# Optimization experiments

Hardware: AMD Instinct MI355X
Metric: run time of the kernel (lower is better)

The kernel has to match this reference:

```python
import jax, jax.numpy as jnp
import numpy as np

N_NODES = 50000
N_EDGES = 1600000
H_DIM = 128
OUT_DIM = 128
N_RELS = 16


def setup_inputs() -> dict:
    key = jax.random.key(0)
    k1, k2, k3, k4, k5, k6 = jax.random.split(key, 6)
    node_ids = jnp.arange(N_NODES, dtype=jnp.int64) if jax.config.jax_enable_x64 else jnp.arange(N_NODES, dtype=jnp.int32)
    src = jax.random.randint(k1, (N_EDGES,), 0, N_NODES, dtype=jnp.int32)
    dst = jax.random.randint(k2, (N_EDGES,), 0, N_NODES, dtype=jnp.int32)
    rel = jax.random.randint(k3, (N_EDGES,), 0, N_RELS, dtype=jnp.int32)
    norm = jax.random.uniform(k4, (N_EDGES, 1), dtype=jnp.float32)
    emb_table = jax.random.normal(k5, (N_NODES, H_DIM), dtype=jnp.float32)
    W = jax.random.normal(k6, (N_RELS, H_DIM, OUT_DIM), dtype=jnp.float32) * (1.0 / np.sqrt(H_DIM))
    return {"node_ids": node_ids, "src": src, "dst": dst, "rel": rel,
            "norm": norm, "emb_table": emb_table, "W": W}


def reference(node_ids, src, dst, rel, norm, emb_table, W):
    # Input layer: embedding lookup on node ids.  [N, h_dim]
    h = emb_table[node_ids]
    n_nodes = emb_table.shape[0]
    # RelGraphConv (full per-relation weight, no basis, no self-loop,
    # activation=None for the single/last layer, dropout inactive at eval):
    # Transform all node features by every relation weight up front
    # (R small, avoids [E, d, o] per-edge weight gather).  [R, N, out]
    h_rel = jnp.einsum('nd,rdo->rno', h, W)
    # Gather per-edge transformed source features, apply edge norm.  [E, out]
    msg = h_rel[rel, src] * norm
    # Scatter-sum messages to destination nodes.  [N, out]
    out = jax.ops.segment_sum(msg, dst, num_segments=n_nodes)
    return out
```

## Files before the change

kernel.cpp:

```cpp
#include <hip/hip_runtime.h>
#include <hip/hip_bf16.h>

#define NN 50000
#define NE 1600000
#define HD 128
#define OD 128
#define NR 16
#define NNP 50176
#define HIST_BLKS 391
#define PREPH_BLKS 6250
#define PREPW_BLKS 1024

typedef __bf16 bf16x8 __attribute__((ext_vector_type(8)));
typedef unsigned short u16x8 __attribute__((ext_vector_type(8)));
typedef float f32x4 __attribute__((ext_vector_type(4)));

__device__ __forceinline__ unsigned short f2bf(float f) {
    union { float f; unsigned int u; } v; v.f = f;
    unsigned int u = v.u;
    u += 0x7FFFu + ((u >> 16) & 1u);
    return (unsigned short)(u >> 16);
}
__device__ __forceinline__ float bflo(unsigned int u) {
    union { unsigned int u; float f; } v; v.u = u << 16; return v.f;
}
__device__ __forceinline__ float bfhi(unsigned int u) {
    union { unsigned int u; float f; } v; v.u = u & 0xFFFF0000u; return v.f;
}

__global__ __launch_bounds__(256) void prep_fused(const int* __restrict__ node_ids,
                                                  const float* __restrict__ emb,
                                                  unsigned short* __restrict__ h_bf,
                                                  const float* __restrict__ W,
                                                  unsigned short* __restrict__ Wt,
                                                  const int* __restrict__ dst,
                                                  int* __restrict__ counts4,
                                                  unsigned short* __restrict__ rank16) {
    const int b = blockIdx.x;
    const int t = threadIdx.x;
    if (b < HIST_BLKS) {
        int t16 = (b * 256 + t) * 16;
        if (t16 >= NE) return;
        int4 d0 = *(const int4*)(dst + t16);
        int4 d1 = *(const int4*)(dst + t16 + 4);
        int4 d2 = *(const int4*)(dst + t16 + 8);
        int4 d3 = *(const int4*)(dst + t16 + 12);
        int r0  = atomicAdd(&counts4[d0.x], 1);
        int r1  = atomicAdd(&counts4[NNP + d0.y], 1);
        int r2  = atomicAdd(&counts4[2 * NNP + d0.z], 1);
        int r3  = atomicAdd(&counts4[3 * NNP + d0.w], 1);
        int r4  = atomicAdd(&counts4[d1.x], 1);
        int r5  = atomicAdd(&counts4[NNP + d1.y], 1);
        int r6  = atomicAdd(&counts4[2 * NNP + d1.z], 1);
        int r7  = atomicAdd(&counts4[3 * NNP + d1.w], 1);
        int r8  = atomicAdd(&counts4[d2.x], 1);
        int r9  = atomicAdd(&counts4[NNP + d2.y], 1);
        int r10 = atomicAdd(&counts4[2 * NNP + d2.z], 1);
        int r11 = atomicAdd(&counts4[3 * NNP + d2.w], 1);
        int r12 = atomicAdd(&counts4[d3.x], 1);
        int r13 = atomicAdd(&counts4[NNP + d3.y], 1);
        int r14 = atomicAdd(&counts4[2 * NNP + d3.z], 1);
        int r15 = atomicAdd(&counts4[3 * NNP + d3.w], 1);
        uint4 pa, pb;
        pa.x = (unsigned int)(r0  & 0xFFFF) | ((unsigned int)r1  << 16);
        pa.y = (unsigned int)(r2  & 0xFFFF) | ((unsigned int)r3  << 16);
        pa.z = (unsigned int)(r4  & 0xFFFF) | ((unsigned int)r5  << 16);
        pa.w = (unsigned int)(r6  & 0xFFFF) | ((unsigned int)r7  << 16);
        pb.x = (unsigned int)(r8  & 0xFFFF) | ((unsigned int)r9  << 16);
        pb.y = (unsigned int)(r10 & 0xFFFF) | ((unsigned int)r11 << 16);
        pb.z = (unsigned int)(r12 & 0xFFFF) | ((unsigned int)r13 << 16);
        pb.w = (unsigned int)(r14 & 0xFFFF) | ((unsigned int)r15 << 16);
        *(uint4*)(rank16 + t16) = pa;
        *(uint4*)(rank16 + t16 + 8) = pb;
    } else if (b < HIST_BLKS + PREPH_BLKS) {
        int gid = (b - HIST_BLKS) * 256 + t;
        int row = gid >> 5;
        int c = (gid & 31) << 2;
        int nid = node_ids[row];
        if (nid < 0) nid = 0; if (nid >= NN) nid = NN - 1;
        float4 v = *(const float4*)(emb + (size_t)nid * HD + c);
        ushort4 o;
        o.x = f2bf(v.x); o.y = f2bf(v.y); o.z = f2bf(v.z); o.w = f2bf(v.w);
        *(ushort4*)(h_bf + (size_t)row * HD + c) = o;
    } else {
        int gid = (b - HIST_BLKS - PREPH_BLKS) * 256 + t;
        int r = gid >> 14;
        int idx = gid & 16383;
        int k = idx >> 7;
        int o = idx & 127;
        Wt[(size_t)r * 16384 + (size_t)o * 128 + k] = f2bf(W[gid]);
    }
}

__global__ __launch_bounds__(256) void gemm_hrel(const unsigned short* __restrict__ h_bf,
                                                 const unsigned short* __restrict__ Wt,
                                                 unsigned short* __restrict__ h_rel) {
    __shared__ unsigned short sA[128][136];
    __shared__ unsigned short sB[128][136];
    const int t = threadIdx.x;
    const int base = blockIdx.x * 128;
    const int rg = blockIdx.y;

    #pragma unroll
    for (int j = 0; j < 8; ++j) {
        int idx = t + j * 256;
        int row = idx >> 4;
        int c8 = (idx & 15) << 3;
        int g = base + row;
        if (g >= NN) g = 0;
        uint4 v = *(const uint4*)(h_bf + (size_t)g * 128 + c8);
        *(uint4*)&sA[row][c8] = v;
    }

    const int lane = t & 63;
    const int w = t >> 6;
    const int wr = w >> 1, wc = w & 1;
    const int l15 = lane & 15, lhi = lane >> 4;

    for (int rr = 0; rr < 4; ++rr) {
        const int r = rg * 4 + rr;
        if (rr > 0) __syncthreads();
        const unsigned short* wp = Wt + ((size_t)r << 14);
        #pragma unroll
        for (int j = 0; j < 8; ++j) {
            int idx = t + j * 256;
            int row = idx >> 4;
            int c8 = (idx & 15) << 3;
            uint4 v = *(const uint4*)(wp + (size_t)row * 128 + c8);
            *(uint4*)&sB[row][c8] = v;
        }
        __syncthreads();

        f32x4 acc[4][4];
        #pragma unroll
        for (int i = 0; i < 4; ++i)
            #pragma unroll
            for (int j = 0; j < 4; ++j)
                acc[i][j] = (f32x4){0.f, 0.f, 0.f, 0.f};

        #pragma unroll
        for (int kt = 0; kt < 4; ++kt) {
            const int ko = kt * 32 + lhi * 8;
            bf16x8 aF[4], bF[4];
            #pragma unroll
            for (int ms = 0; ms < 4; ++ms) {
                u16x8 raw = *(const u16x8*)&sA[wr * 64 + ms * 16 + l15][ko];
                aF[ms] = __builtin_bit_cast(bf16x8, raw);
            }
            #pragma unroll
            for (int nt = 0; nt < 4; ++nt) {
                u16x8 raw = *(const u16x8*)&sB[wc * 64 + nt * 16 + l15][ko];
                bF[nt] = __builtin_bit_cast(bf16x8, raw);
            }
            #pragma unroll
            for (int ms = 0; ms < 4; ++ms)
                #pragma unroll
                for (int nt = 0; nt < 4; ++nt)
                    acc[ms][nt] = __builtin_amdgcn_mfma_f32_16x16x32_bf16(
                        aF[ms], bF[nt], acc[ms][nt], 0, 0, 0);
        }

        #pragma unroll
        for (int ms = 0; ms < 4; ++ms) {
            #pragma unroll
            for (int reg = 0; reg < 4; ++reg) {
                int m = base + wr * 64 + ms * 16 + lhi * 4 + reg;
                if (m < NN) {
                    size_t rowp = ((size_t)r * NN + m) * 128;
                    #pragma unroll
                    for (int nt = 0; nt < 4; ++nt) {
                        int o = wc * 64 + nt * 16 + l15;
                        h_rel[rowp + o] = f2bf(acc[ms][nt][reg]);
                    }
                }
            }
        }
    }
}


__global__ __launch_bounds__(256) void scanA(const int* __restrict__ counts4,
                                             int* __restrict__ blockSums) {
    __shared__ int s[256];
    int t = threadIdx.x;
    int idx = blockIdx.x * 256 + t;
    s[t] = counts4[idx] + counts4[NNP + idx] + counts4[2 * NNP + idx]
         + counts4[3 * NNP + idx];
    __syncthreads();
    for (int off = 128; off > 0; off >>= 1) {
        if (t < off) s[t] += s[t + off];
        __syncthreads();
    }
    if (t == 0) blockSums[blockIdx.x] = s[0];
}

__global__ __launch_bounds__(256) void scanB(int* __restrict__ blockSums) {
    __shared__ int s[256];
    int t = threadIdx.x;
    int v = (t < 196) ? blockSums[t] : 0;
    s[t] = v;
    __syncthreads();
    for (int off = 1; off < 256; off <<= 1) {
        int x = (t >= off) ? s[t - off] : 0;
        __syncthreads();
        s[t] += x;
        __syncthreads();
    }
    if (t < 196) blockSums[t] = s[t] - v;
}

__global__ __launch_bounds__(256) void scanC(int* __restrict__ counts4,
                                             const int* __restrict__ blockSums) {
    __shared__ int s[256];
    int t = threadIdx.x;
    int idx = blockIdx.x * 256 + t;
    int c0 = counts4[idx], c1 = counts4[NNP + idx];
    int c2 = counts4[2 * NNP + idx], c3 = counts4[3 * NNP + idx];
    int v = c0 + c1 + c2 + c3;
    s[t] = v;
    __syncthreads();
    for (int off = 1; off < 256; off <<= 1) {
        int x = (t >= off) ? s[t - off] : 0;
        __syncthreads();
        s[t] += x;
        __syncthreads();
    }
    int st = blockSums[blockIdx.x] + s[t] - v;
    counts4[idx] = st;
    counts4[NNP + idx] = st + c0;
    counts4[2 * NNP + idx] = st + c0 + c1;
    counts4[3 * NNP + idx] = st + c0 + c1 + c2;
}

__global__ __launch_bounds__(256) void scatter_norank(const int* __restrict__ src,
                                                      const int* __restrict__ dst,
                                                      const int* __restrict__ rel,
                                                      const float* __restrict__ norm,
                                                      const int* __restrict__ startS,
                                                      const unsigned short* __restrict__ rank16,
                                                      uint2* __restrict__ recs) {
    int e4 = (blockIdx.x * 256 + threadIdx.x) * 4;
    if (e4 >= NE) return;
    int4 dv = *(const int4*)(dst + e4);
    int4 sv = *(const int4*)(src + e4);
    int4 rv = *(const int4*)(rel + e4);
    float4 nv = *(const float4*)(norm + e4);
    ushort4 rk = *(const ushort4*)(rank16 + e4);
    int p0 = startS[dv.x] + (int)rk.x;
    int p1 = startS[NNP + dv.y] + (int)rk.y;
    int p2 = startS[2 * NNP + dv.z] + (int)rk.z;
    int p3 = startS[3 * NNP + dv.w] + (int)rk.w;
    recs[p0] = make_uint2((unsigned int)(rv.x * NN + sv.x), __float_as_uint(nv.x));
    recs[p1] = make_uint2((unsigned int)(rv.y * NN + sv.y), __float_as_uint(nv.y));
    recs[p2] = make_uint2((unsigned int)(rv.z * NN + sv.z), __float_as_uint(nv.z));
    recs[p3] = make_uint2((unsigned int)(rv.w * NN + sv.w), __float_as_uint(nv.w));
}

__global__ __launch_bounds__(256) void seg_reduce(const int* __restrict__ start,
                                                  const uint2* __restrict__ recs,
                                                  const unsigned int* __restrict__ hb,
                                                  float* __restrict__ out) {
    int d = blockIdx.x * 4 + (threadIdx.x >> 6);
    if (d >= NN) return;
    int lane = threadIdx.x & 63;
    int beg = start[d], end = start[d + 1];
    float a0 = 0.f, a1 = 0.f;
    int i = beg;
    if ((i & 1) && i < end) {
        uint2 rc = recs[i];
        unsigned int u = hb[rc.x * 64u + lane];
        float nm = __uint_as_float(rc.y);
        a0 += bflo(u) * nm;
        a1 += bfhi(u) * nm;
        ++i;
    }
    for (; i + 7 < end; i += 8) {
        uint4 p0 = *(const uint4*)&recs[i];
        uint4 p1 = *(const uint4*)&recs[i + 2];
        uint4 p2 = *(const uint4*)&recs[i + 4];
        uint4 p3 = *(const uint4*)&recs[i + 6];
        unsigned int u0 = hb[p0.x * 64u + lane];
        unsigned int u1 = hb[p0.z * 64u + lane];
        unsigned int u2 = hb[p1.x * 64u + lane];
        unsigned int u3 = hb[p1.z * 64u + lane];
        unsigned int u4 = hb[p2.x * 64u + lane];
        unsigned int u5 = hb[p2.z * 64u + lane];
        unsigned int u6 = hb[p3.x * 64u + lane];
        unsigned int u7 = hb[p3.z * 64u + lane];
        float n0 = __uint_as_float(p0.y), n1 = __uint_as_float(p0.w);
        float n2 = __uint_as_float(p1.y), n3 = __uint_as_float(p1.w);
        float n4 = __uint_as_float(p2.y), n5 = __uint_as_float(p2.w);
        float n6 = __uint_as_float(p3.y), n7 = __uint_as_float(p3.w);
        a0 += bflo(u0) * n0 + bflo(u1) * n1 + bflo(u2) * n2 + bflo(u3) * n3;
        a1 += bfhi(u0) * n0 + bfhi(u1) * n1 + bfhi(u2) * n2 + bfhi(u3) * n3;
        a0 += bflo(u4) * n4 + bflo(u5) * n5 + bflo(u6) * n6 + bflo(u7) * n7;
        a1 += bfhi(u4) * n4 + bfhi(u5) * n5 + bfhi(u6) * n6 + bfhi(u7) * n7;
    }
    for (; i < end; ++i) {
        uint2 rc = recs[i];
        unsigned int u = hb[rc.x * 64u + lane];
        float nm = __uint_as_float(rc.y);
        a0 += bflo(u) * nm;
        a1 += bfhi(u) * nm;
    }
    *(float2*)(out + (size_t)d * 128 + lane * 2) = make_float2(a0, a1);
}


extern "C" void kernel_launch(void* const* d_in, const int* in_sizes, int n_in,
                              void* d_out, int out_size, void* d_ws, size_t ws_size,
                              hipStream_t stream) {
    const int* node_ids = (const int*)d_in[0];
    const int* src      = (const int*)d_in[1];
    const int* dst      = (const int*)d_in[2];
    const int* rel      = (const int*)d_in[3];
    const float* norm   = (const float*)d_in[4];
    const float* emb    = (const float*)d_in[5];
    const float* W      = (const float*)d_in[6];
    float* out = (float*)d_out;

    char* ws = (char*)d_ws;
    unsigned short* h_rel = (unsigned short*)(ws);
    unsigned short* h_bf  = (unsigned short*)(ws + 204800000);
    uint2* recs           = (uint2*)(ws + 204800000);
    unsigned short* Wt    = (unsigned short*)(ws + 217600000);
    int* counts4          = (int*)(ws + 218124288);
    unsigned short* rank16= (unsigned short*)(ws + 218927104);
    int* blockSums        = (int*)(ws + 222127104);

    hipMemsetAsync(counts4, 0, 4 * NNP * sizeof(int), stream);

    prep_fused<<<HIST_BLKS + PREPH_BLKS + PREPW_BLKS, 256, 0, stream>>>(
        node_ids, emb, h_bf, W, Wt, dst, counts4, rank16);
    scanA<<<196, 256, 0, stream>>>(counts4, blockSums);
    scanB<<<1, 256, 0, stream>>>(blockSums);
    scanC<<<196, 256, 0, stream>>>(counts4, blockSums);

    gemm_hrel<<<dim3(391, 4), 256, 0, stream>>>(h_bf, Wt, h_rel);

    scatter_norank<<<(NE / 4 + 255) / 256, 256, 0, stream>>>(src, dst, rel, norm,
                                                             counts4, rank16, recs);

    seg_reduce<<<12500, 256, 0, stream>>>(counts4, recs,
                                          (const unsigned int*)h_rel, out);
}
```

Before: 337.7 us.

## Overlap destination histogram atomics with relation GEMM in one launch

```diff
diff --git a/kernel.cpp b/kernel.cpp
--- a/kernel.cpp
+++ b/kernel.cpp
@@ -7,9 +7,11 @@
 #define OD 128
 #define NR 16
 #define NNP 50176
-#define HIST_BLKS 391
 #define PREPH_BLKS 6250
 #define PREPW_BLKS 1024
+#define HB 64
+#define NCH 100000
+#define GEMM_BLKS 1564
 
 typedef __bf16 bf16x8 __attribute__((ext_vector_type(8)));
 typedef unsigned short u16x8 __attribute__((ext_vector_type(8)));
@@ -28,52 +30,15 @@
     union { unsigned int u; float f; } v; v.u = u & 0xFFFF0000u; return v.f;
 }
 
-__global__ __launch_bounds__(256) void prep_fused(const int* __restrict__ node_ids,
-                                                  const float* __restrict__ emb,
-                                                  unsigned short* __restrict__ h_bf,
-                                                  const float* __restrict__ W,
-                                                  unsigned short* __restrict__ Wt,
-                                                  const int* __restrict__ dst,
-                                                  int* __restrict__ counts4,
-                                                  unsigned short* __restrict__ rank16) {
+__global__ __launch_bounds__(256) void prep_hw(const int* __restrict__ node_ids,
+                                               const float* __restrict__ emb,
+                                               unsigned short* __restrict__ h_bf,
+                                               const float* __restrict__ W,
+                                               unsigned short* __restrict__ Wt) {
     const int b = blockIdx.x;
     const int t = threadIdx.x;
-    if (b < HIST_BLKS) {
-        int t16 = (b * 256 + t) * 16;
-        if (t16 >= NE) return;
-        int4 d0 = *(const int4*)(dst + t16);
-        int4 d1 = *(const int4*)(dst + t16 + 4);
-        int4 d2 = *(const int4*)(dst + t16 + 8);
-        int4 d3 = *(const int4*)(dst + t16 + 12);
-        int r0  = atomicAdd(&counts4[d0.x], 1);
-        int r1  = atomicAdd(&counts4[NNP + d0.y], 1);
-        int r2  = atomicAdd(&counts4[2 * NNP + d0.z], 1);
-        int r3  = atomicAdd(&counts4[3 * NNP + d0.w], 1);
-        int r4  = atomicAdd(&counts4[d1.x], 1);
-        int r5  = atomicAdd(&counts4[NNP + d1.y], 1);
-        int r6  = atomicAdd(&counts4[2 * NNP + d1.z], 1);
-        int r7  = atomicAdd(&counts4[3 * NNP + d1.w], 1);
-        int r8  = atomicAdd(&counts4[d2.x], 1);
-        int r9  = atomicAdd(&counts4[NNP + d2.y], 1);
-        int r10 = atomicAdd(&counts4[2 * NNP + d2.z], 1);
-        int r11 = atomicAdd(&counts4[3 * NNP + d2.w], 1);
-        int r12 = atomicAdd(&counts4[d3.x], 1);
-        int r13 = atomicAdd(&counts4[NNP + d3.y], 1);
-        int r14 = atomicAdd(&counts4[2 * NNP + d3.z], 1);
-        int r15 = atomicAdd(&counts4[3 * NNP + d3.w], 1);
-        uint4 pa, pb;
-        pa.x = (unsigned int)(r0  & 0xFFFF) | ((unsigned int)r1  << 16);
-        pa.y = (unsigned int)(r2  & 0xFFFF) | ((unsigned int)r3  << 16);
-        pa.z = (unsigned int)(r4  & 0xFFFF) | ((unsigned int)r5  << 16);
-        pa.w = (unsigned int)(r6  & 0xFFFF) | ((unsigned int)r7  << 16);
-        pb.x = (unsigned int)(r8  & 0xFFFF) | ((unsigned int)r9  << 16);
-        pb.y = (unsigned int)(r10 & 0xFFFF) | ((unsigned int)r11 << 16);
-        pb.z = (unsigned int)(r12 & 0xFFFF) | ((unsigned int)r13 << 16);
-        pb.w = (unsigned int)(r14 & 0xFFFF) | ((unsigned int)r15 << 16);
-        *(uint4*)(rank16 + t16) = pa;
-        *(uint4*)(rank16 + t16 + 8) = pb;
-    } else if (b < HIST_BLKS + PREPH_BLKS) {
-        int gid = (b - HIST_BLKS) * 256 + t;
+    if (b < PREPH_BLKS) {
+        int gid = b * 256 + t;
         int row = gid >> 5;
         int c = (gid & 31) << 2;
         int nid = node_ids[row];
@@ -83,7 +48,7 @@
         o.x = f2bf(v.x); o.y = f2bf(v.y); o.z = f2bf(v.z); o.w = f2bf(v.w);
         *(ushort4*)(h_bf + (size_t)row * HD + c) = o;
     } else {
-        int gid = (b - HIST_BLKS - PREPH_BLKS) * 256 + t;
+        int gid = (b - PREPH_BLKS) * 256 + t;
         int r = gid >> 14;
         int idx = gid & 16383;
         int k = idx >> 7;
@@ -92,23 +57,69 @@
     }
 }
 
-__global__ __launch_bounds__(256) void gemm_hrel(const unsigned short* __restrict__ h_bf,
-                                                 const unsigned short* __restrict__ Wt,
-                                                 unsigned short* __restrict__ h_rel) {
+__global__ __launch_bounds__(256) void gemm_hist(
+        const unsigned short* __restrict__ h_bf,
+        const unsigned short* __restrict__ Wt,
+        unsigned short* __restrict__ h_rel,
+        const int* __restrict__ dst,
+        int* __restrict__ counts4,
+        unsigned short* __restrict__ rank16) {
     __shared__ unsigned short sA[128][136];
     __shared__ unsigned short sB[128][136];
     const int t = threadIdx.x;
-    const int base = blockIdx.x * 128;
-    const int rg = blockIdx.y;
+
+    if (blockIdx.x < HB) {
+        int tid = blockIdx.x * 256 + t;
+        for (int c = tid; c < NCH; c += HB * 256) {
+            int e16 = c * 16;
+            int4 d0 = *(const int4*)(dst + e16);
+            int4 d1 = *(const int4*)(dst + e16 + 4);
+            int4 d2 = *(const int4*)(dst + e16 + 8);
+            int4 d3 = *(const int4*)(dst + e16 + 12);
+            int r0  = atomicAdd(&counts4[d0.x], 1);
+            int r1  = atomicAdd(&counts4[NNP + d0.y], 1);
+            int r2  = atomicAdd(&counts4[2 * NNP + d0.z], 1);
+            int r3  = atomicAdd(&counts4[3 * NNP + d0.w], 1);
+            int r4  = atomicAdd(&counts4[d1.x], 1);
+            int r5  = atomicAdd(&counts4[NNP + d1.y], 1);
+            int r6  = atomicAdd(&counts4[2 * NNP + d1.z], 1);
+            int r7  = atomicAdd(&counts4[3 * NNP + d1.w], 1);
+            int r8  = atomicAdd(&counts4[d2.x], 1);
+            int r9  = atomicAdd(&counts4[NNP + d2.y], 1);
+            int r10 = atomicAdd(&counts4[2 * NNP + d2.z], 1);
+            int r11 = atomicAdd(&counts4[3 * NNP + d2.w], 1);
+            int r12 = atomicAdd(&counts4[d3.x], 1);
+            int r13 = atomicAdd(&counts4[NNP + d3.y], 1);
+            int r14 = atomicAdd(&counts4[2 * NNP + d3.z], 1);
+            int r15 = atomicAdd(&counts4[3 * NNP + d3.w], 1);
+            uint4 pa, pb;
+            pa.x = (unsigned int)(r0  & 0xFFFF) | ((unsigned int)r1  << 16);
+            pa.y = (unsigned int)(r2  & 0xFFFF) | ((unsigned int)r3  << 16);
+            pa.z = (unsigned int)(r4  & 0xFFFF) | ((unsigned int)r5  << 16);
+            pa.w = (unsigned int)(r6  & 0xFFFF) | ((unsigned int)r7  << 16);
+            pb.x = (unsigned int)(r8  & 0xFFFF) | ((unsigned int)r9  << 16);
+            pb.y = (unsigned int)(r10 & 0xFFFF) | ((unsigned int)r11 << 16);
+            pb.z = (unsigned int)(r12 & 0xFFFF) | ((unsigned int)r13 << 16);
+            pb.w = (unsigned int)(r14 & 0xFFFF) | ((unsigned int)r15 << 16);
+            *(uint4*)(rank16 + e16) = pa;
+            *(uint4*)(rank16 + e16 + 8) = pb;
+        }
+        return;
+    }
+
+    const int g = blockIdx.x - HB;
+    const int tile = g % 391;
+    const int rg = g / 391;
+    const int base = tile * 128;
 
     #pragma unroll
     for (int j = 0; j < 8; ++j) {
         int idx = t + j * 256;
         int row = idx >> 4;
         int c8 = (idx & 15) << 3;
-        int g = base + row;
-        if (g >= NN) g = 0;
-        uint4 v = *(const uint4*)(h_bf + (size_t)g * 128 + c8);
+        int gg = base + row;
+        if (gg >= NN) gg = 0;
+        uint4 v = *(const uint4*)(h_bf + (size_t)gg * 128 + c8);
         *(uint4*)&sA[row][c8] = v;
     }
 
@@ -330,14 +341,15 @@
 
     hipMemsetAsync(counts4, 0, 4 * NNP * sizeof(int), stream);
 
-    prep_fused<<<HIST_BLKS + PREPH_BLKS + PREPW_BLKS, 256, 0, stream>>>(
-        node_ids, emb, h_bf, W, Wt, dst, counts4, rank16);
+    prep_hw<<<PREPH_BLKS + PREPW_BLKS, 256, 0, stream>>>(node_ids, emb, h_bf, W, Wt);
+
+    gemm_hist<<<HB + GEMM_BLKS, 256, 0, stream>>>(h_bf, Wt, h_rel,
+                                                  dst, counts4, rank16);
+
     scanA<<<196, 256, 0, stream>>>(counts4, blockSums);
     scanB<<<1, 256, 0, stream>>>(blockSums);
     scanC<<<196, 256, 0, stream>>>(counts4, blockSums);
 
-    gemm_hrel<<<dim3(391, 4), 256, 0, stream>>>(h_bf, Wt, h_rel);
-
     scatter_norank<<<(NE / 4 + 255) / 256, 256, 0, stream>>>(src, dst, rel, norm,
                                                              counts4, rank16, recs);
 
```

Measured after the change: 328.5 us. -2.7%, faster.
